# Kernel tuning notes

Measured on AMD Instinct MI355X. Metric: run time of the kernel, lower is better.

## Reference

```python
import jax, jax.numpy as jnp
import numpy as np

X_GRID, Y_GRID = 192, 132
HW = X_GRID * Y_GRID            # 25344
NUM_PROP = 500
NUM_CLS = 6
RADIUS = 10
L_WIN = (2 * RADIUS + 1) ** 2   # 441
D = 128
N_HEADS = 8
D_HEAD = D // N_HEADS
VX, VY = 0.64, 0.64             # feature_map_stride * voxel_size
PC_X0, PC_Y0 = -61.44, -42.24


def _bev_pos():
    # create_2D_grid: linspace(0, size-1, size) + 0.5, meshgrid 'ij', flatten row-major
    bx, by = jnp.meshgrid(jnp.arange(X_GRID, dtype=jnp.float32) + 0.5,
                          jnp.arange(Y_GRID, dtype=jnp.float32) + 0.5, indexing='ij')
    return jnp.stack([bx.reshape(-1), by.reshape(-1)], axis=-1)[None]  # [1, HW, 2]


def conv2d(x, w, b):
    y = jax.lax.conv_general_dilated(x, w, (1, 1), 'SAME',
                                     dimension_numbers=('NCHW', 'OIHW', 'NCHW'))
    return y + b[None, :, None, None]


def maxpool3_valid(x):
    return jax.lax.reduce_window(x, -jnp.inf, jax.lax.max,
                                 (1, 1, 3, 3), (1, 1, 1, 1), 'VALID')


def layer_norm(x, g, b, eps=1e-5):
    m = jnp.mean(x, axis=-1, keepdims=True)
    v = jnp.var(x, axis=-1, keepdims=True)
    return (x - m) * jax.lax.rsqrt(v + eps) * g + b


def pos_emb(p, W1, b1, W2, b2):
    return jax.nn.relu(p @ W1 + b1) @ W2 + b2


def _forward(inputs, W_shared, b_shared, W_hm, b_hm, W_cls, b_cls,
             W_pos1, b_pos1, W_pos2, b_pos2, Wq, bq, Wk, bk, Wv, bv, Wo, bo,
             ln1_g, ln1_b, ln2_g, ln2_b, W_ff1, b_ff1, W_ff2, b_ff2,
             W_center, b_center, W_height, b_height, W_dim, b_dim,
             W_rot, b_rot, W_iou, b_iou, W_hm2, b_hm2):
    x = jnp.transpose(inputs, (0, 1, 3, 2))          # [B,C,192,132]
    B = x.shape[0]
    lidar_feat = jax.nn.relu(conv2d(x, W_shared, b_shared))   # [B,128,192,132]
    lff = lidar_feat.reshape(B, D, HW)

    dense_heatmap = conv2d(lidar_feat, W_hm, b_hm)            # [B,6,192,132]
    heatmap = jax.nn.sigmoid(jax.lax.stop_gradient(dense_heatmap))  # detached in original

    # local-max NMS: 3x3 maxpool on inner region, zeros at border; classes 3..5 bypass NMS
    inner = maxpool3_valid(heatmap)
    local_max = jnp.pad(inner, ((0, 0), (0, 0), (1, 1), (1, 1)))
    local_max = local_max.at[:, 3:6].set(heatmap[:, 3:6])
    hm = heatmap * (heatmap == local_max)

    # threshold + top-k proposals (replaces nonzero+pad+MySortImpe plugin)
    hm_flat = hm.reshape(B, NUM_CLS * HW)
    vals = jnp.where(hm_flat > 0.01, hm_flat, 0.0)
    _, top = jax.lax.top_k(vals, NUM_PROP)            # [B,500]
    cls = top // HW
    sp = top % HW

    query_feat = jnp.take_along_axis(lff, sp[:, None, :], axis=2)  # [B,128,500]
    oh = jax.nn.one_hot(cls, NUM_CLS, dtype=lff.dtype)             # [B,500,6]
    query_feat = query_feat + jnp.einsum('bpc,oc->bop', oh, W_cls) + b_cls[None, :, None]

    bev_pos = jnp.broadcast_to(_bev_pos(), (B, HW, 2))
    query_pos = jnp.take_along_axis(bev_pos, sp[:, :, None], axis=1)  # [B,500,2]

    # windowed key indices (faithful to original //x_grid, %y_grid arithmetic)
    rng = jnp.arange(-RADIUS, RADIUS + 1)
    rx, ry = jnp.meshgrid(rng, rng, indexing='ij')
    kx = (sp // X_GRID)[:, :, None, None] + rx[None, None]
    ky = (sp % Y_GRID)[:, :, None, None] + ry[None, None]
    key_idx = kx.reshape(B, NUM_PROP, L_WIN) * X_GRID + ky.reshape(B, NUM_PROP, L_WIN)
    key_mask = (key_idx < 0) | (key_idx >= HW)
    key_idx = jnp.clip(key_idx, 0, HW - 1)

    key_feat = jnp.take_along_axis(lff, key_idx.reshape(B, 1, -1), axis=2)
    key_feat = key_feat.reshape(B, D, NUM_PROP, L_WIN)
    key_pos = jnp.take_along_axis(bev_pos, key_idx.reshape(B, -1, 1), axis=1)
    key_pos = key_pos.reshape(B, NUM_PROP, L_WIN, 2)

    # decoder: cross-attention of each proposal over its 441-key window
    N = B * NUM_PROP
    q = query_feat.transpose(0, 2, 1).reshape(N, D)
    k = key_feat.transpose(0, 2, 3, 1).reshape(N, L_WIN, D)
    mask = key_mask.reshape(N, L_WIN)
    qpe = pos_emb(query_pos.reshape(N, 2), W_pos1, b_pos1, W_pos2, b_pos2)
    kpe = pos_emb(key_pos.reshape(N, L_WIN, 2), W_pos1, b_pos1, W_pos2, b_pos2)

    qh = ((q + qpe) @ Wq + bq).reshape(N, N_HEADS, D_HEAD)
    kh = ((k + kpe) @ Wk + bk).reshape(N, L_WIN, N_HEADS, D_HEAD)
    vh = (k @ Wv + bv).reshape(N, L_WIN, N_HEADS, D_HEAD)
    scores = jnp.einsum('nhd,nlhd->nhl', qh, kh) / np.float32(np.sqrt(D_HEAD))
    scores = jnp.where(mask[:, None, :], jnp.float32(-1e9), scores)
    attn = jax.nn.softmax(scores, axis=-1)
    ctx = jnp.einsum('nhl,nlhd->nhd', attn, vh).reshape(N, D)
    x1 = layer_norm(q + ctx @ Wo + bo, ln1_g, ln1_b)
    ff = jax.nn.relu(x1 @ W_ff1 + b_ff1) @ W_ff2 + b_ff2
    x2 = layer_norm(x1 + ff, ln2_g, ln2_b)

    qf = x2.reshape(B, NUM_PROP, D).transpose(0, 2, 1)   # [B,128,500]
    head = lambda W, b: jnp.einsum('bcp,oc->bop', qf, W) + b[None, :, None]
    center = head(W_center, b_center) + query_pos.transpose(0, 2, 1)
    height = head(W_height, b_height)
    dim = head(W_dim, b_dim)
    rot = head(W_rot, b_rot)
    iou = head(W_iou, b_iou)
    hm2 = head(W_hm2, b_hm2)

    # get_bboxes / decode_bbox
    score = jax.nn.sigmoid(hm2)                          # [B,6,500]
    _ = (iou + 1.0) * 0.5                                # computed, unused (as in original)
    final_preds = jnp.argmax(score, axis=1).astype(score.dtype)
    final_scores = jnp.max(score, axis=1)
    cx = center[:, 0:1] * VX + PC_X0
    cy = center[:, 1:2] * VY + PC_Y0
    dim = jnp.exp(dim)
    height = height - dim[:, 2:3] * 0.5
    rot = jnp.arctan(rot[:, 0:1] / (rot[:, 1:2] + 1e-6))
    box = jnp.concatenate([cx, cy, height, dim, rot,
                           final_preds[:, None, :], final_scores[:, None, :]], axis=1)
    return box.transpose(0, 2, 1)                        # [B,500,9]


def setup_inputs() -> dict:
    key = jax.random.key(0)
    ks = jax.random.split(key, 20)
    r = lambda k, shape, s=0.02: jax.random.normal(k, shape, dtype=jnp.float32) * s
    z = lambda n: jnp.zeros((n,), dtype=jnp.float32)
    o = lambda n: jnp.ones((n,), dtype=jnp.float32)
    return {
        'inputs': jax.random.normal(ks[0], (1, 256, 132, 192), dtype=jnp.float32),
        'W_shared': r(ks[1], (128, 256, 3, 3)), 'b_shared': z(128),
        'W_hm': r(ks[2], (6, 128, 3, 3)), 'b_hm': z(6),
        'W_cls': r(ks[3], (128, 6)), 'b_cls': z(128),
        'W_pos1': r(ks[4], (2, 128)), 'b_pos1': z(128),
        'W_pos2': r(ks[5], (128, 128)), 'b_pos2': z(128),
        'Wq': r(ks[6], (128, 128)), 'bq': z(128),
        'Wk': r(ks[7], (128, 128)), 'bk': z(128),
        'Wv': r(ks[8], (128, 128)), 'bv': z(128),
        'Wo': r(ks[9], (128, 128)), 'bo': z(128),
        'ln1_g': o(128), 'ln1_b': z(128),
        'ln2_g': o(128), 'ln2_b': z(128),
        'W_ff1': r(ks[10], (128, 256)), 'b_ff1': z(256),
        'W_ff2': r(ks[11], (256, 128)), 'b_ff2': z(128),
        'W_center': r(ks[12], (2, 128)), 'b_center': z(2),
        'W_height': r(ks[13], (1, 128)), 'b_height': z(1),
        'W_dim': r(ks[14], (3, 128)), 'b_dim': z(3),
        'W_rot': r(ks[15], (2, 128)), 'b_rot': z(2),
        'W_iou': r(ks[16], (1, 128)), 'b_iou': z(1),
        'W_hm2': r(ks[17], (6, 128)), 'b_hm2': z(6),
    }


def reference(inputs, W_shared, b_shared, W_hm, b_hm, W_cls, b_cls,
              W_pos1, b_pos1, W_pos2, b_pos2, Wq, bq, Wk, bk, Wv, bv, Wo, bo,
              ln1_g, ln1_b, ln2_g, ln2_b, W_ff1, b_ff1, W_ff2, b_ff2,
              W_center, b_center, W_height, b_height, W_dim, b_dim,
              W_rot, b_rot, W_iou, b_iou, W_hm2, b_hm2):
    return _forward(inputs, W_shared, b_shared, W_hm, b_hm, W_cls, b_cls,
                    W_pos1, b_pos1, W_pos2, b_pos2, Wq, bq, Wk, bk, Wv, bv, Wo, bo,
                    ln1_g, ln1_b, ln2_g, ln2_b, W_ff1, b_ff1, W_ff2, b_ff2,
                    W_center, b_center, W_height, b_height, W_dim, b_dim,
                    W_rot, b_rot, W_iou, b_iou, W_hm2, b_hm2)
```

## Files before the change

kernel.cpp:

```cpp
#include <hip/hip_runtime.h>
#include <math.h>
#include <float.h>

#define XG 192
#define YG 132
#define HW 25344
#define NCLS 6
#define NPROP 500
#define LWIN 441
#define CAP 2048

static __device__ __forceinline__ int imin(int a,int b){return a<b?a:b;}
static __device__ __forceinline__ int imax(int a,int b){return a>b?a:b;}

__device__ __forceinline__ void gl_lds16(const float* gp, float* lp){
  __builtin_amdgcn_global_load_lds(
      (const __attribute__((address_space(1))) unsigned int*)gp,
      (__attribute__((address_space(3))) unsigned int*)lp,
      16, 0, 0);
}

__global__ __launch_bounds__(256) void k_wt(const float* __restrict__ Ws,
                                            const float* __restrict__ Whm,
                                            const float* __restrict__ Wq,
                                            const float* __restrict__ Wp2,
                                            const float* __restrict__ Wo,
                                            const float* __restrict__ Wf1,
                                            const float* __restrict__ Wf2,
                                            float* __restrict__ WT,
                                            float* __restrict__ W6,
                                            float* __restrict__ WQT,
                                            float* __restrict__ WP2T,
                                            float* __restrict__ WOT,
                                            float* __restrict__ WF1T,
                                            float* __restrict__ WF2T,
                                            int* __restrict__ Z){
  int t = blockIdx.x*256 + threadIdx.x;
  if (t < 294912){
    int oc = t & 127, m = t >> 7;
    WT[t] = Ws[(size_t)oc*2304 + m];
  }
  if (t < 6912){
    int c = t & 127, row = t >> 7;
    int cls = row / 9, tap = row % 9;
    W6[t] = Whm[(size_t)cls*1152 + c*9 + tap];
  }
  if (t < 16384){
    int k = t & 127, c = t >> 7;
    WQT[t]  = Wq [(size_t)k*128 + c];
    WP2T[t] = Wp2[(size_t)k*128 + c];
    WOT[t]  = Wo [(size_t)k*128 + c];
  }
  if (t < 32768){
    { int k = t & 127, o = t >> 7;  WF1T[t] = Wf1[(size_t)k*256 + o]; }
    { int k = t & 255, c = t >> 8;  WF2T[t] = Wf2[(size_t)k*128 + c]; }
  }
  if (t < 65568) Z[t] = 0;
}

__global__ __launch_bounds__(256, 4) void k_conv1(const float* __restrict__ IN,
                                                  const float* __restrict__ WT,
                                                  float* __restrict__ O0, float* __restrict__ O1,
                                                  float* __restrict__ O2, float* __restrict__ O3){
  const int b  = blockIdx.x;
  const int g  = blockIdx.y;
  const int i0 = (b % 3) * 64;
  const int j  = b / 3;
  const int tid = threadIdx.x;
  const int wv  = tid >> 6;
  const int oc0 = (tid & 31) * 4;
  const int pxs = tid >> 5;
  __shared__ float wlds[4608];
  __shared__ float hlds[816];
  float4 acc[8];
  #pragma unroll
  for (int px=0;px<8;++px) acc[px] = make_float4(0.f,0.f,0.f,0.f);
  const int C0g = g*64;
  for (int q=0; q<16; ++q){
    __syncthreads();
    const float* wchunk = WT + (size_t)(C0g + q*4)*1152;
    #pragma unroll
    for (int r=0; r<4; ++r)
      gl_lds16(wchunk + (size_t)(r*256 + tid)*4, wlds + (size_t)(r*256 + wv*64)*4);
    if (wv < 2)
      gl_lds16(wchunk + (size_t)(1024 + tid)*4, wlds + (size_t)(1024 + wv*64)*4);
    for (int e=tid; e<792; e+=256){
      int cc = e/198, rem = e%198, r = rem/66, ii = rem%66;
      int gj = j-1+r, gi = i0-1+ii;
      float v = 0.f;
      if ((unsigned)gj < 132u && (unsigned)gi < 192u)
        v = IN[(size_t)(C0g+q*4+cc)*25344 + gj*192 + gi];
      hlds[cc*204 + r*68 + ii] = v;
    }
    __syncthreads();
    for (int cc=0; cc<4; ++cc){
      const float* hb = hlds + cc*204 + pxs*8;
      const float* wb = wlds + cc*1152 + oc0;
      float a[3][10];
      #pragma unroll
      for (int r=0;r<3;++r)
        #pragma unroll
        for (int v=0; v<10; ++v) a[r][v] = hb[r*68 + v];
      #pragma unroll
      for (int kh=0;kh<3;++kh){
        #pragma unroll
        for (int kw=0;kw<3;++kw){
          float4 w = *(const float4*)(wb + (kh*3+kw)*128);
          #pragma unroll
          for (int px=0;px<8;++px){
            float act = a[kw][px+kh];
            acc[px].x += act*w.x;
            acc[px].y += act*w.y;
            acc[px].z += act*w.z;
            acc[px].w += act*w.w;
          }
        }
      }
    }
  }
  float* dst = (g==0)?O0:((g==1)?O1:((g==2)?O2:O3));
  #pragma unroll
  for (int px=0;px<8;++px){
    int p = (i0 + pxs*8 + px)*132 + j;
    *(float4*)(dst + (size_t)p*128 + oc0) = acc[px];
  }
}

__global__ __launch_bounds__(256) void k_cadd(float* __restrict__ LFF,
                                              const float* __restrict__ P1,
                                              const float* __restrict__ P2,
                                              const float* __restrict__ P3,
                                              const float* __restrict__ bias){
  int t = blockIdx.x*256 + threadIdx.x;
  float4 a = ((const float4*)LFF)[t];
  float4 b = ((const float4*)P1)[t];
  float4 c = ((const float4*)P2)[t];
  float4 d = ((const float4*)P3)[t];
  float4 bs = ((const float4*)bias)[t & 31];
  float4 r;
  r.x = fmaxf(a.x+b.x+c.x+d.x+bs.x, 0.f);
  r.y = fmaxf(a.y+b.y+c.y+d.y+bs.y, 0.f);
  r.z = fmaxf(a.z+b.z+c.z+d.z+bs.z, 0.f);
  r.w = fmaxf(a.w+b.w+c.w+d.w+bs.w, 0.f);
  ((float4*)LFF)[t] = r;
}

__global__ __launch_bounds__(256) void k_mid(const float* __restrict__ LFF,
                                             const float* __restrict__ W1, const float* __restrict__ b1,
                                             const float* __restrict__ W2, const float* __restrict__ b2,
                                             const float* __restrict__ Wk, const float* __restrict__ bk,
                                             const float* __restrict__ Wv, const float* __restrict__ bv,
                                             float* __restrict__ KK, float* __restrict__ VV,
                                             const float* __restrict__ W6, const float* __restrict__ bhm,
                                             float* __restrict__ HMS){
  __shared__ float smem[12288];
  const int tid = threadIdx.x;
  const int wv4 = tid >> 6;
  if (blockIdx.x < 792){
    float* hs   = smem;
    float* sf   = smem + 4096;
    float* wbuf = smem + 8192;
    const int p0 = blockIdx.x*32;
    for (int e=tid; e<4096; e+=256){
      int k = e>>5, px = e&31;
      int p = p0+px;
      float bx = (float)(p/132)+0.5f, by = (float)(p%132)+0.5f;
      hs[k*32+px] = fmaxf(bx*W1[k] + by*W1[128+k] + b1[k], 0.f);
    }
    for (int e=tid; e<4096; e+=256){
      int px = e>>7, k = e&127;
      sf[k*32+px] = LFF[(size_t)(p0+px)*128 + k];
    }
    const int pxg = tid & 15, ocg = tid >> 4;
    const int px0 = pxg*2, oc0 = ocg*8;
    float accA[2][8];
    #pragma unroll
    for (int r=0;r<2;++r)
      #pragma unroll
      for (int u=0;u<8;++u) accA[r][u]=0.f;
    for (int c0=0; c0<128; c0+=32){
      __syncthreads();
      const float* wsrc = W2 + (size_t)c0*128;
      #pragma unroll
      for (int r=0;r<4;++r)
        gl_lds16(wsrc + (size_t)(r*256+tid)*4, wbuf + (size_t)(r*256+wv4*64)*4);
      __syncthreads();
      #pragma unroll 2
      for (int k=0;k<32;++k){
        float a0 = hs[(c0+k)*32+px0], a1 = hs[(c0+k)*32+px0+1];
        const float4* w = (const float4*)(wbuf + (size_t)k*128 + oc0);
        float4 w0 = w[0], w1 = w[1];
        accA[0][0]+=a0*w0.x; accA[0][1]+=a0*w0.y; accA[0][2]+=a0*w0.z; accA[0][3]+=a0*w0.w;
        accA[0][4]+=a0*w1.x; accA[0][5]+=a0*w1.y; accA[0][6]+=a0*w1.z; accA[0][7]+=a0*w1.w;
        accA[1][0]+=a1*w0.x; accA[1][1]+=a1*w0.y; accA[1][2]+=a1*w0.z; accA[1][3]+=a1*w0.w;
        accA[1][4]+=a1*w1.x; accA[1][5]+=a1*w1.y; accA[1][6]+=a1*w1.z; accA[1][7]+=a1*w1.w;
      }
    }
    __syncthreads();
    #pragma unroll
    for (int u=0;u<8;++u){
      float bb = b2[oc0+u];
      hs[(oc0+u)*32+px0]   = sf[(oc0+u)*32+px0]   + accA[0][u] + bb;
      hs[(oc0+u)*32+px0+1] = sf[(oc0+u)*32+px0+1] + accA[1][u] + bb;
    }
    float accK[2][8], accV[2][8];
    #pragma unroll
    for (int u=0;u<8;++u){
      float k0 = bk[oc0+u], v0 = bv[oc0+u];
      accK[0][u]=k0; accK[1][u]=k0; accV[0][u]=v0; accV[1][u]=v0;
    }
    for (int c0=0; c0<128; c0+=16){
      __syncthreads();
      #pragma unroll
      for (int r=0;r<2;++r){
        gl_lds16(Wk + (size_t)c0*128 + (size_t)(r*256+tid)*4, wbuf + (size_t)(r*256+wv4*64)*4);
        gl_lds16(Wv + (size_t)c0*128 + (size_t)(r*256+tid)*4, wbuf + 2048 + (size_t)(r*256+wv4*64)*4);
      }
      __syncthreads();
      #pragma unroll 2
      for (int k=0;k<16;++k){
        int kk = c0+k;
        float s0 = hs[kk*32+px0], s1 = hs[kk*32+px0+1];
        float f0 = sf[kk*32+px0], f1 = sf[kk*32+px0+1];
        const float4* wkp = (const float4*)(wbuf + (size_t)k*128 + oc0);
        const float4* wvp = (const float4*)(wbuf + 2048 + (size_t)k*128 + oc0);
        float4 k0v = wkp[0], k1v = wkp[1], v0v = wvp[0], v1v = wvp[1];
        accK[0][0]+=s0*k0v.x; accK[0][1]+=s0*k0v.y; accK[0][2]+=s0*k0v.z; accK[0][3]+=s0*k0v.w;
        accK[0][4]+=s0*k1v.x; accK[0][5]+=s0*k1v.y; accK[0][6]+=s0*k1v.z; accK[0][7]+=s0*k1v.w;
        accK[1][0]+=s1*k0v.x; accK[1][1]+=s1*k0v.y; accK[1][2]+=s1*k0v.z; accK[1][3]+=s1*k0v.w;
        accK[1][4]+=s1*k1v.x; accK[1][5]+=s1*k1v.y; accK[1][6]+=s1*k1v.z; accK[1][7]+=s1*k1v.w;
        accV[0][0]+=f0*v0v.x; accV[0][1]+=f0*v0v.y; accV[0][2]+=f0*v0v.z; accV[0][3]+=f0*v0v.w;
        accV[0][4]+=f0*v1v.x; accV[0][5]+=f0*v1v.y; accV[0][6]+=f0*v1v.z; accV[0][7]+=f0*v1v.w;
        accV[1][0]+=f1*v0v.x; accV[1][1]+=f1*v0v.y; accV[1][2]+=f1*v0v.z; accV[1][3]+=f1*v0v.w;
        accV[1][4]+=f1*v1v.x; accV[1][5]+=f1*v1v.y; accV[1][6]+=f1*v1v.z; accV[1][7]+=f1*v1v.w;
      }
    }
    #pragma unroll
    for (int r=0;r<2;++r){
      int p = p0+px0+r;
      float4* oK = (float4*)(KK + (size_t)p*128 + oc0);
      float4* oV = (float4*)(VV + (size_t)p*128 + oc0);
      float4 t0, t1;
      t0.x=accK[r][0]; t0.y=accK[r][1]; t0.z=accK[r][2]; t0.w=accK[r][3];
      t1.x=accK[r][4]; t1.y=accK[r][5]; t1.z=accK[r][6]; t1.w=accK[r][7];
      oK[0]=t0; oK[1]=t1;
      t0.x=accV[r][0]; t0.y=accV[r][1]; t0.z=accV[r][2]; t0.w=accV[r][3];
      t1.x=accV[r][4]; t1.y=accV[r][5]; t1.z=accV[r][6]; t1.w=accV[r][7];
      oV[0]=t0; oV[1]=t1;
    }
  } else {
    float* w6s = smem;
    float* red = smem + 8192;
    for (int e=tid; e<6912; e+=256) w6s[e] = W6[e];
    __syncthreads();
    int lane = tid & 63, wave = tid >> 6;
    int p = (blockIdx.x - 792)*64 + lane;
    int i = p/132, j = p%132;
    float acc[6] = {0.f,0.f,0.f,0.f,0.f,0.f};
    int cbase = wave*32;
    #pragma unroll
    for (int kh=0; kh<3; ++kh){
      int gi = i+kh-1;
      if ((unsigned)gi >= 192u) continue;
      #pragma unroll
      for (int kw=0; kw<3; ++kw){
        int gj = j+kw-1;
        if ((unsigned)gj >= 132u) continue;
        const float* row = LFF + (size_t)(gi*132+gj)*128 + cbase;
        int tap = kh*3+kw;
        #pragma unroll
        for (int cq=0; cq<8; ++cq){
          float4 v = *(const float4*)(row + cq*4);
          #pragma unroll
          for (int cls=0; cls<6; ++cls){
            float4 wv = *(const float4*)(w6s + (size_t)(cls*9+tap)*128 + cbase + cq*4);
            acc[cls] += v.x*wv.x + v.y*wv.y + v.z*wv.z + v.w*wv.w;
          }
        }
      }
    }
    __syncthreads();
    #pragma unroll
    for (int c=0;c<6;++c) red[(wave*6+c)*64 + lane] = acc[c];
    __syncthreads();
    if (wave==0){
      #pragma unroll
      for (int c=0;c<6;++c){
        float s = red[c*64+lane] + red[(6+c)*64+lane] + red[(12+c)*64+lane] + red[(18+c)*64+lane] + bhm[c];
        HMS[(size_t)c*HW + p] = 1.f/(1.f+expf(-s));
      }
    }
  }
}

__global__ __launch_bounds__(256) void k_nms(const float* __restrict__ HMS,
                                             float* __restrict__ VALS,
                                             int* __restrict__ HIST){
  int t = blockIdx.x*256 + threadIdx.x;
  int c = t / HW, p = t % HW;
  int i = p/132, j = p%132;
  float h = HMS[t];
  float v;
  if (c < 3){
    v = 0.f;
    if (i>=1 && i<=190 && j>=1 && j<=130){
      float m = -1e30f;
      #pragma unroll
      for (int di=-1;di<=1;++di)
        #pragma unroll
        for (int dj=-1;dj<=1;++dj)
          m = fmaxf(m, HMS[(size_t)c*HW + (i+di)*132 + (j+dj)]);
      if (h == m) v = h;
    }
  } else v = h;
  if (!(v > 0.01f)) v = 0.f;
  VALS[t] = v;
  if (v > 0.f) atomicAdd(HIST + (__float_as_uint(v)>>16), 1);
}

__global__ __launch_bounds__(1024) void k_scan(const int* __restrict__ HIST, int* __restrict__ SCAN){
  __shared__ int part[1024];
  __shared__ int gsel;
  int t = threadIdx.x;
  int s = 0, base = t*64;
  for (int u=0;u<64;++u) s += HIST[base+u];
  part[t] = s;
  __syncthreads();
  for (int off=1; off<1024; off<<=1){
    int add = (t+off < 1024) ? part[t+off] : 0;
    __syncthreads();
    part[t] += add;
    __syncthreads();
  }
  int total = part[0];
  int mineI = part[t];
  int nextI = (t < 1023) ? part[t+1] : 0;
  if (mineI >= NPROP && nextI < NPROP) gsel = t;
  if (t == 0 && total < NPROP) gsel = -1;
  __syncthreads();
  int g = gsel;
  if (g < 0){
    if (t==0){ SCAN[0] = 0; SCAN[1] = total; }
    return;
  }
  int cumG = (g < 1023) ? part[g+1] : 0;
  if (t < 64){
    int x = HIST[g*64 + t];
    #pragma unroll
    for (int off=1; off<64; off<<=1){
      int y = __shfl_down(x, off);
      x += (t + off < 64) ? y : 0;
    }
    int Snext = __shfl_down(x, 1);
    int incl  = cumG + x;
    int nextc = (t==63) ? cumG : cumG + Snext;
    if (incl >= NPROP && nextc < NPROP){
      SCAN[0] = g*64 + t;
      SCAN[1] = nextc;
    }
  }
}

__global__ __launch_bounds__(256) void k_collect(const float* __restrict__ VALS,
                                                 const int* __restrict__ SCAN,
                                                 int* __restrict__ CNT,
                                                 float* __restrict__ CV, int* __restrict__ CI){
  int t = blockIdx.x*256 + threadIdx.x;
  float v = VALS[t];
  int bstar = SCAN[0];
  if (v > 0.f && (int)(__float_as_uint(v)>>16) >= bstar){
    int pos = atomicAdd(CNT, 1);
    if (pos < CAP){ CV[pos] = v; CI[pos] = t; }
  }
}

__global__ __launch_bounds__(1024) void k_sort(const float* __restrict__ CV, const int* __restrict__ CI,
                                               const int* __restrict__ CNT,
                                               int* __restrict__ TOPS, int* __restrict__ TOPC){
  __shared__ float sv[CAP];
  __shared__ int   si[CAP];
  int tid = threadIdx.x;
  int M = imin(CNT[0], CAP);
  for (int i=tid; i<CAP; i+=1024){
    if (i < M){ sv[i] = CV[i]; si[i] = CI[i]; }
    else      { sv[i] = -1.f;  si[i] = 0x7fffffff; }
  }
  __syncthreads();
  for (int k=2; k<=CAP; k<<=1){
    for (int j=k>>1; j>0; j>>=1){
      for (int i=tid; i<CAP; i+=1024){
        int p = i ^ j;
        if (p > i){
          bool up = ((i & k) == 0);
          float va = sv[i], vb = sv[p];
          int ia = si[i], ib = si[p];
          bool aFirst = (va > vb) || (va == vb && ia < ib);
          bool bFirst = (vb > va) || (vb == va && ib < ia);
          bool doswap = up ? bFirst : aFirst;
          if (doswap){ sv[i]=vb; sv[p]=va; si[i]=ib; si[p]=ia; }
        }
      }
      __syncthreads();
    }
  }
  for (int t=tid; t<NPROP; t+=1024){
    int idx = imin(si[t], NCLS*HW - 1);
    TOPC[t] = idx / HW;
    TOPS[t] = idx % HW;
  }
}

__global__ __launch_bounds__(256) void k_attn(const float* __restrict__ KK, const float* __restrict__ VV,
                                              const float* __restrict__ LFF,
                                              const int* __restrict__ TOPS, const int* __restrict__ TOPC,
                                              const float* __restrict__ Wcls, const float* __restrict__ bcls,
                                              const float* __restrict__ pW1, const float* __restrict__ pb1,
                                              const float* __restrict__ WP2T, const float* __restrict__ pb2,
                                              const float* __restrict__ WQT, const float* __restrict__ bq,
                                              const float* __restrict__ WOT, const float* __restrict__ bo,
                                              const float* __restrict__ g1, const float* __restrict__ b1,
                                              const float* __restrict__ WF1T, const float* __restrict__ bf1,
                                              const float* __restrict__ WF2T, const float* __restrict__ bf2,
                                              const float* __restrict__ g2, const float* __restrict__ b2,
                                              const float* __restrict__ Wc, const float* __restrict__ bc,
                                              const float* __restrict__ Wh, const float* __restrict__ bh,
                                              const float* __restrict__ Wd, const float* __restrict__ bd,
                                              const float* __restrict__ Wr, const float* __restrict__ br,
                                              const float* __restrict__ Whm2, const float* __restrict__ bhm2,
                                              float* __restrict__ out){
  int n = blockIdx.x, tid = threadIdx.x;
  __shared__ __align__(16) float qhL[128];
  __shared__ float sc[8*441];
  __shared__ int   kiL[441];
  __shared__ __align__(16) float ctxL[128];
  __shared__ float xL[128];
  __shared__ float hidL[256];
  __shared__ float sumsL[8];
  __shared__ float stat[2];
  __shared__ float dots[16];
  int sp = TOPS[n];
  int cls = TOPC[n];
  const int kb64 = (tid>>7)*64, c128 = tid&127;
  float qreg = 0.f;
  if (tid < 128){
    float qx = (float)(sp/132)+0.5f, qy = (float)(sp%132)+0.5f;
    ctxL[tid] = fmaxf(qx*pW1[tid] + qy*pW1[128+tid] + pb1[tid], 0.f);
    qreg = LFF[(size_t)sp*128+tid] + Wcls[tid*6+cls] + bcls[tid];
  }
  __syncthreads();
  {
    const float4* wp = (const float4*)(WP2T + (size_t)c128*128 + kb64);
    float pe = 0.f;
    #pragma unroll
    for (int k4=0;k4<16;++k4){
      float4 w = wp[k4]; int kb = kb64 + k4*4;
      pe += ctxL[kb]*w.x + ctxL[kb+1]*w.y + ctxL[kb+2]*w.z + ctxL[kb+3]*w.w;
    }
    sc[tid] = pe;
  }
  __syncthreads();
  if (tid < 128) xL[tid] = qreg + pb2[tid] + sc[tid] + sc[tid+128];
  __syncthreads();
  {
    const float4* wp = (const float4*)(WQT + (size_t)c128*128 + kb64);
    float qh = 0.f;
    #pragma unroll
    for (int k4=0;k4<16;++k4){
      float4 w = wp[k4]; int kb = kb64 + k4*4;
      qh += xL[kb]*w.x + xL[kb+1]*w.y + xL[kb+2]*w.z + xL[kb+3]*w.w;
    }
    sc[tid] = qh;
  }
  __syncthreads();
  if (tid < 128) qhL[tid] = bq[tid] + sc[tid] + sc[tid+128];
  __syncthreads();
  int spx = sp/192, spy = sp%132;
  for (int l = tid; l < 441; l += 256){
    int a = l/21, bb = l%21;
    int kidx = (spx + a - 10)*192 + (spy + bb - 10);
    bool msk = (kidx < 0) || (kidx >= HW);
    int kc = imin(imax(kidx,0), HW-1);
    kiL[l] = kc;
    const float4* kk4 = (const float4*)(KK + (size_t)kc*128);
    const float4* qh4 = (const float4*)qhL;
    #pragma unroll
    for (int hh=0; hh<8; ++hh){
      float acc = 0.f;
      #pragma unroll
      for (int d4=0; d4<4; ++d4){
        float4 kv = kk4[hh*4+d4]; float4 qv = qh4[hh*4+d4];
        acc += kv.x*qv.x + kv.y*qv.y + kv.z*qv.z + kv.w*qv.w;
      }
      sc[hh*441+l] = msk ? -1e9f : acc*0.25f;
    }
  }
  __syncthreads();
  int wave = tid>>6, lane = tid&63;
  for (int hh = wave; hh < 8; hh += 4){
    float mx = -3.0e38f;
    for (int l = lane; l < 441; l += 64) mx = fmaxf(mx, sc[hh*441+l]);
    #pragma unroll
    for (int off=32; off; off>>=1) mx = fmaxf(mx, __shfl_xor(mx, off));
    float sum = 0.f;
    for (int l = lane; l < 441; l += 64){
      float e = __expf(sc[hh*441+l] - mx);
      sc[hh*441+l] = e; sum += e;
    }
    #pragma unroll
    for (int off=32; off; off>>=1) sum += __shfl_xor(sum, off);
    if (lane==0) sumsL[hh] = sum;
  }
  __syncthreads();
  for (int hh = wave; hh < 8; hh += 4){
    float a[16];
    #pragma unroll
    for (int d=0; d<16; ++d) a[d]=0.f;
    for (int l = lane; l < 441; l += 64){
      float w = sc[hh*441+l];
      const float4* vv4 = (const float4*)(VV + (size_t)kiL[l]*128 + hh*16);
      #pragma unroll
      for (int d4=0; d4<4; ++d4){
        float4 v = vv4[d4];
        a[d4*4+0]+=w*v.x; a[d4*4+1]+=w*v.y; a[d4*4+2]+=w*v.z; a[d4*4+3]+=w*v.w;
      }
    }
    #pragma unroll
    for (int d=0; d<16; ++d){
      #pragma unroll
      for (int off=32; off; off>>=1) a[d] += __shfl_xor(a[d], off);
    }
    if (lane==0){
      float inv = 1.f/sumsL[hh];
      #pragma unroll
      for (int d=0; d<16; ++d) ctxL[hh*16+d] = a[d]*inv;
    }
  }
  __syncthreads();
  {
    const float4* wp = (const float4*)(WOT + (size_t)c128*128 + kb64);
    float acc = 0.f;
    #pragma unroll
    for (int k4=0;k4<16;++k4){
      float4 w = wp[k4]; int kb = kb64 + k4*4;
      acc += ctxL[kb]*w.x + ctxL[kb+1]*w.y + ctxL[kb+2]*w.z + ctxL[kb+3]*w.w;
    }
    sc[tid] = acc;
  }
  __syncthreads();
  float x1v = 0.f;
  if (tid < 128){
    x1v = qreg + bo[tid] + sc[tid] + sc[tid+128];
    xL[tid] = x1v;
  }
  __syncthreads();
  if (tid < 64){
    float u0 = xL[tid], u1 = xL[tid+64];
    float s = u0+u1, s2 = u0*u0+u1*u1;
    #pragma unroll
    for (int off=32; off; off>>=1){ s += __shfl_xor(s, off); s2 += __shfl_xor(s2, off); }
    if (tid==0){ float mean = s*(1.f/128.f); float var = s2*(1.f/128.f) - mean*mean;
      stat[0]=mean; stat[1]=rsqrtf(var + 1e-5f); }
  }
  __syncthreads();
  if (tid < 128) xL[tid] = (x1v - stat[0])*stat[1]*g1[tid] + b1[tid];
  __syncthreads();
  {
    const float4* wp = (const float4*)(WF1T + (size_t)tid*128);
    float hv = bf1[tid];
    #pragma unroll 8
    for (int k4=0;k4<32;++k4){
      float4 w = wp[k4]; int kb = k4*4;
      hv += xL[kb]*w.x + xL[kb+1]*w.y + xL[kb+2]*w.z + xL[kb+3]*w.w;
    }
    hidL[tid] = fmaxf(hv, 0.f);
  }
  __syncthreads();
  {
    int kb0 = (tid>>7)*128;
    const float4* wp = (const float4*)(WF2T + (size_t)c128*256 + kb0);
    float acc = 0.f;
    #pragma unroll 8
    for (int k4=0;k4<32;++k4){
      float4 w = wp[k4]; int kb = kb0 + k4*4;
      acc += hidL[kb]*w.x + hidL[kb+1]*w.y + hidL[kb+2]*w.z + hidL[kb+3]*w.w;
    }
    sc[tid] = acc;
  }
  __syncthreads();
  float x2v = 0.f;
  if (tid < 128) x2v = xL[tid] + bf2[tid] + sc[tid] + sc[tid+128];
  __syncthreads();
  if (tid < 128) hidL[tid] = x2v;
  __syncthreads();
  if (tid < 64){
    float u0 = hidL[tid], u1 = hidL[tid+64];
    float s = u0+u1, s2 = u0*u0+u1*u1;
    #pragma unroll
    for (int off=32; off; off>>=1){ s += __shfl_xor(s, off); s2 += __shfl_xor(s2, off); }
    if (tid==0){ float mean = s*(1.f/128.f); float var = s2*(1.f/128.f) - mean*mean;
      stat[0]=mean; stat[1]=rsqrtf(var + 1e-5f); }
  }
  __syncthreads();
  if (tid < 128) xL[tid] = (x2v - stat[0])*stat[1]*g2[tid] + b2[tid];
  __syncthreads();
  if (tid < 14){
    const float* Wp; float bb;
    if (tid < 2)      { Wp = Wc + tid*128;        bb = bc[tid];      }
    else if (tid < 3) { Wp = Wh;                  bb = bh[0];        }
    else if (tid < 6) { Wp = Wd + (tid-3)*128;    bb = bd[tid-3];    }
    else if (tid < 8) { Wp = Wr + (tid-6)*128;    bb = br[tid-6];    }
    else              { Wp = Whm2 + (tid-8)*128;  bb = bhm2[tid-8];  }
    float acc = bb;
    for (int k=0;k<128;++k) acc += xL[k]*Wp[k];
    dots[tid] = acc;
  }
  __syncthreads();
  if (tid == 0){
    float qpx = (float)(sp/132)+0.5f, qpy = (float)(sp%132)+0.5f;
    float cx = (dots[0]+qpx)*0.64f - 61.44f;
    float cy = (dots[1]+qpy)*0.64f - 42.24f;
    float e0 = expf(dots[3]), e1 = expf(dots[4]), e2 = expf(dots[5]);
    float hgt = dots[2] - e2*0.5f;
    float rot = atanf(dots[6]/(dots[7] + 1e-6f));
    float bestv = -1.f; int bestc = 0;
    #pragma unroll
    for (int m=0;m<6;++m){
      float s = 1.f/(1.f + expf(-dots[8+m]));
      if (s > bestv){ bestv = s; bestc = m; }
    }
    float* o = out + (size_t)n*9;
    o[0]=cx; o[1]=cy; o[2]=hgt; o[3]=e0; o[4]=e1; o[5]=e2; o[6]=rot;
    o[7]=(float)bestc; o[8]=bestv;
  }
}

extern "C" void kernel_launch(void* const* d_in, const int* in_sizes, int n_in,
                              void* d_out, int out_size, void* d_ws, size_t ws_size,
                              hipStream_t stream){
  (void)in_sizes; (void)n_in; (void)out_size;
  const float* IN   = (const float*)d_in[0];
  const float* Wsh  = (const float*)d_in[1];
  const float* bsh  = (const float*)d_in[2];
  const float* Whm  = (const float*)d_in[3];
  const float* bhm  = (const float*)d_in[4];
  const float* Wcls = (const float*)d_in[5];
  const float* bcls = (const float*)d_in[6];
  const float* Wp1  = (const float*)d_in[7];
  const float* bp1  = (const float*)d_in[8];
  const float* Wp2  = (const float*)d_in[9];
  const float* bp2  = (const float*)d_in[10];
  const float* Wq   = (const float*)d_in[11];
  const float* bq   = (const float*)d_in[12];
  const float* Wk   = (const float*)d_in[13];
  const float* bk   = (const float*)d_in[14];
  const float* Wv   = (const float*)d_in[15];
  const float* bv   = (const float*)d_in[16];
  const float* Wo   = (const float*)d_in[17];
  const float* bo   = (const float*)d_in[18];
  const float* g1   = (const float*)d_in[19];
  const float* b1   = (const float*)d_in[20];
  const float* g2   = (const float*)d_in[21];
  const float* b2   = (const float*)d_in[22];
  const float* Wf1  = (const float*)d_in[23];
  const float* bf1  = (const float*)d_in[24];
  const float* Wf2  = (const float*)d_in[25];
  const float* bf2  = (const float*)d_in[26];
  const float* Wc   = (const float*)d_in[27];
  const float* bc   = (const float*)d_in[28];
  const float* Wh   = (const float*)d_in[29];
  const float* bh   = (const float*)d_in[30];
  const float* Wd   = (const float*)d_in[31];
  const float* bd   = (const float*)d_in[32];
  const float* Wr   = (const float*)d_in[33];
  const float* br   = (const float*)d_in[34];
  const float* Whm2 = (const float*)d_in[37];
  const float* bhm2 = (const float*)d_in[38];
  float* out = (float*)d_out;
  float* W = (float*)d_ws;

  const size_t N_LFF  = (size_t)HW*128;
  const size_t OFF_LFF  = 0;
  const size_t OFF_PE   = OFF_LFF + N_LFF;
  const size_t OFF_KK   = OFF_PE + N_LFF;
  const size_t OFF_VV   = OFF_KK + N_LFF;
  const size_t OFF_WT   = OFF_VV + N_LFF;
  const size_t OFF_WHMT = OFF_WT + 294912;
  const size_t OFF_HMS  = OFF_WHMT + 6912;
  const size_t OFF_VALS = OFF_HMS + 152064;
  const size_t OFF_HIST = OFF_VALS + 152064;
  const size_t OFF_SCAN = OFF_HIST + 65536;
  const size_t OFF_CNT  = OFF_SCAN + 16;
  const size_t OFF_CV   = OFF_CNT + 16;
  const size_t OFF_CI   = OFF_CV + CAP;
  const size_t OFF_TOPS = OFF_CI + CAP;
  const size_t OFF_TOPC = OFF_TOPS + 512;
  const size_t OFF_WQT  = OFF_TOPC + 512;
  const size_t OFF_WP2T = OFF_WQT + 16384;
  const size_t OFF_WOT  = OFF_WP2T + 16384;
  const size_t OFF_WF1T = OFF_WOT + 16384;
  const size_t OFF_WF2T = OFF_WF1T + 32768;
  const size_t TOTAL    = OFF_WF2T + 32768;
  if (ws_size < TOTAL*sizeof(float)) return;

  k_wt    <<<1152, 256, 0, stream>>>(Wsh, Whm, Wq, Wp2, Wo, Wf1, Wf2,
                                     W+OFF_WT, W+OFF_WHMT,
                                     W+OFF_WQT, W+OFF_WP2T, W+OFF_WOT, W+OFF_WF1T, W+OFF_WF2T,
                                     (int*)(W+OFF_HIST));
  k_conv1 <<<dim3(396,4), 256, 0, stream>>>(IN, W+OFF_WT, W+OFF_LFF, W+OFF_PE, W+OFF_KK, W+OFF_VV);
  k_cadd  <<<3168, 256, 0, stream>>>(W+OFF_LFF, W+OFF_PE, W+OFF_KK, W+OFF_VV, bsh);
  k_mid   <<<1188, 256, 0, stream>>>(W+OFF_LFF, Wp1, bp1, Wp2, bp2, Wk, bk, Wv, bv,
                                     W+OFF_KK, W+OFF_VV, W+OFF_WHMT, bhm, W+OFF_HMS);
  k_nms   <<<594,  256, 0, stream>>>(W+OFF_HMS, W+OFF_VALS, (int*)(W+OFF_HIST));
  k_scan  <<<1,   1024, 0, stream>>>((const int*)(W+OFF_HIST), (int*)(W+OFF_SCAN));
  k_collect<<<594, 256, 0, stream>>>(W+OFF_VALS, (const int*)(W+OFF_SCAN),
                                     (int*)(W+OFF_CNT), W+OFF_CV, (int*)(W+OFF_CI));
  k_sort  <<<1,   1024, 0, stream>>>(W+OFF_CV, (const int*)(W+OFF_CI), (const int*)(W+OFF_CNT),
                                     (int*)(W+OFF_TOPS), (int*)(W+OFF_TOPC));
  k_attn  <<<500,  256, 0, stream>>>(W+OFF_KK, W+OFF_VV, W+OFF_LFF,
                                     (const int*)(W+OFF_TOPS), (const int*)(W+OFF_TOPC),
                                     Wcls, bcls, Wp1, bp1, W+OFF_WP2T, bp2, W+OFF_WQT, bq,
                                     W+OFF_WOT, bo, g1, b1, W+OFF_WF1T, bf1, W+OFF_WF2T, bf2, g2, b2,
                                     Wc, bc, Wh, bh, Wd, bd, Wr, br, Whm2, bhm2, out);
}
```

Baseline: 583.3 us.

## Run shared 3x3 conv on bf16 MFMA with three-way split precision

Replaces the FP32 FMA direct convolution, which was split over four channel groups with partial sums, with one implicit-GEMM kernel on bf16 MFMA 16x16x32 instructions. Inputs and weights are each split into three bf16 parts, and six cross-product MFMAs per tile keep accuracy close to FP32. Bias and ReLU are fused into the epilogue, which removes the separate partial-sum add kernel and the three extra HW×128 buffers. In exchange it adds activation splitting inside the kernel, more block-level syncs per channel chunk and tap, and lower occupancy.

```diff
diff --git a/kernel.cpp b/kernel.cpp
--- a/kernel.cpp
+++ b/kernel.cpp
@@ -10,6 +10,10 @@
 #define LWIN 441
 #define CAP 2048
 
+typedef unsigned short ushort_t;
+typedef __attribute__((ext_vector_type(8))) short bf8v;
+typedef __attribute__((ext_vector_type(4))) float f4v;
+
 static __device__ __forceinline__ int imin(int a,int b){return a<b?a:b;}
 static __device__ __forceinline__ int imax(int a,int b){return a>b?a:b;}
 
@@ -18,6 +22,20 @@
       (const __attribute__((address_space(1))) unsigned int*)gp,
       (__attribute__((address_space(3))) unsigned int*)lp,
       16, 0, 0);
+}
+__device__ __forceinline__ void gl_lds16u(const ushort_t* gp, ushort_t* lp){
+  __builtin_amdgcn_global_load_lds(
+      (const __attribute__((address_space(1))) unsigned int*)gp,
+      (__attribute__((address_space(3))) unsigned int*)lp,
+      16, 0, 0);
+}
+
+__device__ __forceinline__ ushort_t f2bf(float x){
+  unsigned u = __float_as_uint(x);
+  return (ushort_t)((u + 0x7FFFu + ((u>>16)&1u)) >> 16);
+}
+__device__ __forceinline__ float bf2f(ushort_t h){
+  return __uint_as_float(((unsigned)h)<<16);
 }
 
 __global__ __launch_bounds__(256) void k_wt(const float* __restrict__ Ws,
@@ -27,18 +45,32 @@
                                             const float* __restrict__ Wo,
                                             const float* __restrict__ Wf1,
                                             const float* __restrict__ Wf2,
-                                            float* __restrict__ WT,
                                             float* __restrict__ W6,
                                             float* __restrict__ WQT,
                                             float* __restrict__ WP2T,
                                             float* __restrict__ WOT,
                                             float* __restrict__ WF1T,
                                             float* __restrict__ WF2T,
+                                            ushort_t* __restrict__ BQ0,
+                                            ushort_t* __restrict__ BQ1,
+                                            ushort_t* __restrict__ BQ2,
                                             int* __restrict__ Z){
   int t = blockIdx.x*256 + threadIdx.x;
   if (t < 294912){
-    int oc = t & 127, m = t >> 7;
-    WT[t] = Ws[(size_t)oc*2304 + m];
+    int kl = t & 31;
+    int rest = t >> 5;
+    int n = rest & 127;
+    int tc = rest >> 7;
+    int tap = tc >> 3, chunk = tc & 7;
+    int c = chunk*32 + kl;
+    float v = Ws[(size_t)n*2304 + c*9 + tap];
+    ushort_t h0 = f2bf(v);
+    float r1 = v - bf2f(h0);
+    ushort_t h1 = f2bf(r1);
+    float r2 = r1 - bf2f(h1);
+    ushort_t h2 = f2bf(r2);
+    size_t dst = (size_t)tc*5120 + n*40 + kl;
+    BQ0[dst] = h0; BQ1[dst] = h1; BQ2[dst] = h2;
   }
   if (t < 6912){
     int c = t & 127, row = t >> 7;
@@ -58,91 +90,130 @@
   if (t < 65568) Z[t] = 0;
 }
 
-__global__ __launch_bounds__(256, 4) void k_conv1(const float* __restrict__ IN,
-                                                  const float* __restrict__ WT,
-                                                  float* __restrict__ O0, float* __restrict__ O1,
-                                                  float* __restrict__ O2, float* __restrict__ O3){
+__global__ __launch_bounds__(256, 3) void k_conv1(const float* __restrict__ IN,
+                                                  const ushort_t* __restrict__ BQ0,
+                                                  const ushort_t* __restrict__ BQ1,
+                                                  const ushort_t* __restrict__ BQ2,
+                                                  const float* __restrict__ bias,
+                                                  float* __restrict__ LFF){
   const int b  = blockIdx.x;
-  const int g  = blockIdx.y;
   const int i0 = (b % 3) * 64;
   const int j  = b / 3;
   const int tid = threadIdx.x;
-  const int wv  = tid >> 6;
-  const int oc0 = (tid & 31) * 4;
-  const int pxs = tid >> 5;
-  __shared__ float wlds[4608];
-  __shared__ float hlds[816];
-  float4 acc[8];
+  const int w    = tid >> 6;
+  const int lane = tid & 63;
+  const int l15  = lane & 15, quad = lane >> 4;
+  __shared__ __align__(16) ushort_t SM[23280];
+  ushort_t* As0 = SM;
+  ushort_t* As1 = SM + 2640;
+  ushort_t* As2 = SM + 5280;
+  ushort_t* Bs0 = SM + 7920;
+  ushort_t* Bs1 = SM + 13040;
+  ushort_t* Bs2 = SM + 18160;
+  f4v acc[4][2];
   #pragma unroll
-  for (int px=0;px<8;++px) acc[px] = make_float4(0.f,0.f,0.f,0.f);
-  const int C0g = g*64;
-  for (int q=0; q<16; ++q){
-    __syncthreads();
-    const float* wchunk = WT + (size_t)(C0g + q*4)*1152;
-    #pragma unroll
-    for (int r=0; r<4; ++r)
-      gl_lds16(wchunk + (size_t)(r*256 + tid)*4, wlds + (size_t)(r*256 + wv*64)*4);
-    if (wv < 2)
-      gl_lds16(wchunk + (size_t)(1024 + tid)*4, wlds + (size_t)(1024 + wv*64)*4);
-    for (int e=tid; e<792; e+=256){
-      int cc = e/198, rem = e%198, r = rem/66, ii = rem%66;
-      int gj = j-1+r, gi = i0-1+ii;
-      float v = 0.f;
-      if ((unsigned)gj < 132u && (unsigned)gi < 192u)
-        v = IN[(size_t)(C0g+q*4+cc)*25344 + gj*192 + gi];
-      hlds[cc*204 + r*68 + ii] = v;
-    }
-    __syncthreads();
-    for (int cc=0; cc<4; ++cc){
-      const float* hb = hlds + cc*204 + pxs*8;
-      const float* wb = wlds + cc*1152 + oc0;
-      float a[3][10];
-      #pragma unroll
-      for (int r=0;r<3;++r)
-        #pragma unroll
-        for (int v=0; v<10; ++v) a[r][v] = hb[r*68 + v];
-      #pragma unroll
-      for (int kh=0;kh<3;++kh){
-        #pragma unroll
-        for (int kw=0;kw<3;++kw){
-          float4 w = *(const float4*)(wb + (kh*3+kw)*128);
-          #pragma unroll
-          for (int px=0;px<8;++px){
-            float act = a[kw][px+kh];
-            acc[px].x += act*w.x;
-            acc[px].y += act*w.y;
-            acc[px].z += act*w.z;
-            acc[px].w += act*w.w;
+  for (int mq=0;mq<4;++mq)
+    #pragma unroll
+    for (int nt=0;nt<2;++nt) acc[mq][nt] = (f4v){0.f,0.f,0.f,0.f};
+
+  for (int chunk=0; chunk<8; ++chunk){
+    for (int kw=0; kw<3; ++kw){
+      __syncthreads();
+      {
+        int gj = j - 1 + kw;
+        bool jok = (unsigned)gj < 132u;
+        for (int e = tid; e < 2112; e += 256){
+          int c = e / 66, ii = e - c*66;
+          int gi = i0 - 1 + ii;
+          float v = 0.f;
+          if (jok && (unsigned)gi < 192u)
+            v = IN[(size_t)(chunk*32 + c)*25344 + gj*192 + gi];
+          ushort_t h0 = f2bf(v);
+          float r1 = v - bf2f(h0);
+          ushort_t h1 = f2bf(r1);
+          float r2 = r1 - bf2f(h1);
+          ushort_t h2 = f2bf(r2);
+          int a = ii*40 + c;
+          As0[a] = h0; As1[a] = h1; As2[a] = h2;
+        }
+      }
+      for (int kh=0; kh<3; ++kh){
+        if (kh > 0) __syncthreads();
+        {
+          int tc = (kh*3 + kw)*8 + chunk;
+          const ushort_t* s0 = BQ0 + (size_t)tc*5120;
+          const ushort_t* s1 = BQ1 + (size_t)tc*5120;
+          const ushort_t* s2 = BQ2 + (size_t)tc*5120;
+          gl_lds16u(s0 + (size_t)tid*8,       Bs0 + (size_t)(w*64)*8);
+          gl_lds16u(s0 + (size_t)(256+tid)*8, Bs0 + (size_t)(256 + w*64)*8);
+          gl_lds16u(s1 + (size_t)tid*8,       Bs1 + (size_t)(w*64)*8);
+          gl_lds16u(s1 + (size_t)(256+tid)*8, Bs1 + (size_t)(256 + w*64)*8);
+          gl_lds16u(s2 + (size_t)tid*8,       Bs2 + (size_t)(w*64)*8);
+          gl_lds16u(s2 + (size_t)(256+tid)*8, Bs2 + (size_t)(256 + w*64)*8);
+          if (tid < 128){
+            gl_lds16u(s0 + (size_t)(512+tid)*8, Bs0 + (size_t)(512 + w*64)*8);
+            gl_lds16u(s1 + (size_t)(512+tid)*8, Bs1 + (size_t)(512 + w*64)*8);
+            gl_lds16u(s2 + (size_t)(512+tid)*8, Bs2 + (size_t)(512 + w*64)*8);
           }
         }
-      }
-    }
-  }
-  float* dst = (g==0)?O0:((g==1)?O1:((g==2)?O2:O3));
+        __syncthreads();
+        bf8v A0[4], A1[4], A2[4];
+        #pragma unroll
+        for (int mq=0; mq<4; ++mq){
+          int off = (mq*16 + l15 + kh)*40 + quad*8;
+          A0[mq] = *(const bf8v*)&As0[off];
+          A1[mq] = *(const bf8v*)&As1[off];
+          A2[mq] = *(const bf8v*)&As2[off];
+        }
+        bf8v B0[2], B1[2], B2[2];
+        #pragma unroll
+        for (int ntl=0; ntl<2; ++ntl){
+          int off = ((w*2+ntl)*16 + l15)*40 + quad*8;
+          B0[ntl] = *(const bf8v*)&Bs0[off];
+          B1[ntl] = *(const bf8v*)&Bs1[off];
+          B2[ntl] = *(const bf8v*)&Bs2[off];
+        }
+        #pragma unroll
+        for (int mq=0;mq<4;++mq){
+          #pragma unroll
+          for (int ntl=0;ntl<2;++ntl){
+            f4v c = acc[mq][ntl];
+            c = __builtin_amdgcn_mfma_f32_16x16x32_bf16(A0[mq], B0[ntl], c, 0,0,0);
+            c = __builtin_amdgcn_mfma_f32_16x16x32_bf16(A0[mq], B1[ntl], c, 0,0,0);
+            c = __builtin_amdgcn_mfma_f32_16x16x32_bf16(A1[mq], B0[ntl], c, 0,0,0);
+            c = __builtin_amdgcn_mfma_f32_16x16x32_bf16(A0[mq], B2[ntl], c, 0,0,0);
+            c = __builtin_amdgcn_mfma_f32_16x16x32_bf16(A1[mq], B1[ntl], c, 0,0,0);
+            c = __builtin_amdgcn_mfma_f32_16x16x32_bf16(A2[mq], B0[ntl], c, 0,0,0);
+            acc[mq][ntl] = c;
+          }
+        }
+      }
+    }
+  }
+  __syncthreads();
+  float* Cs = (float*)SM;
   #pragma unroll
-  for (int px=0;px<8;++px){
-    int p = (i0 + pxs*8 + px)*132 + j;
-    *(float4*)(dst + (size_t)p*128 + oc0) = acc[px];
-  }
-}
-
-__global__ __launch_bounds__(256) void k_cadd(float* __restrict__ LFF,
-                                              const float* __restrict__ P1,
-                                              const float* __restrict__ P2,
-                                              const float* __restrict__ P3,
-                                              const float* __restrict__ bias){
-  int t = blockIdx.x*256 + threadIdx.x;
-  float4 a = ((const float4*)LFF)[t];
-  float4 b = ((const float4*)P1)[t];
-  float4 c = ((const float4*)P2)[t];
-  float4 d = ((const float4*)P3)[t];
-  float4 bs = ((const float4*)bias)[t & 31];
-  float4 r;
-  r.x = fmaxf(a.x+b.x+c.x+d.x+bs.x, 0.f);
-  r.y = fmaxf(a.y+b.y+c.y+d.y+bs.y, 0.f);
-  r.z = fmaxf(a.z+b.z+c.z+d.z+bs.z, 0.f);
-  r.w = fmaxf(a.w+b.w+c.w+d.w+bs.w, 0.f);
-  ((float4*)LFF)[t] = r;
+  for (int mq=0;mq<4;++mq)
+    #pragma unroll
+    for (int ntl=0;ntl<2;++ntl)
+      #pragma unroll
+      for (int r=0;r<4;++r){
+        int m = mq*16 + quad*4 + r;
+        int oc = (w*2+ntl)*16 + l15;
+        Cs[m*128 + oc] = acc[mq][ntl][r];
+      }
+  __syncthreads();
+  for (int e = tid; e < 2048; e += 256){
+    int m = e >> 5, ocq = e & 31;
+    float4 v = *(float4*)&Cs[m*128 + ocq*4];
+    float4 bs = *(const float4*)&bias[ocq*4];
+    v.x = fmaxf(v.x + bs.x, 0.f);
+    v.y = fmaxf(v.y + bs.y, 0.f);
+    v.z = fmaxf(v.z + bs.z, 0.f);
+    v.w = fmaxf(v.w + bs.w, 0.f);
+    int p = (i0 + m)*132 + j;
+    *(float4*)&LFF[(size_t)p*128 + ocq*4] = v;
+  }
 }
 
 __global__ __launch_bounds__(256) void k_mid(const float* __restrict__ LFF,
@@ -680,12 +751,10 @@
 
   const size_t N_LFF  = (size_t)HW*128;
   const size_t OFF_LFF  = 0;
-  const size_t OFF_PE   = OFF_LFF + N_LFF;
-  const size_t OFF_KK   = OFF_PE + N_LFF;
+  const size_t OFF_KK   = OFF_LFF + N_LFF;
   const size_t OFF_VV   = OFF_KK + N_LFF;
-  const size_t OFF_WT   = OFF_VV + N_LFF;
-  const size_t OFF_WHMT = OFF_WT + 294912;
-  const size_t OFF_HMS  = OFF_WHMT + 6912;
+  const size_t OFF_W6   = OFF_VV + N_LFF;
+  const size_t OFF_HMS  = OFF_W6 + 6912;
   const size_t OFF_VALS = OFF_HMS + 152064;
   const size_t OFF_HIST = OFF_VALS + 152064;
   const size_t OFF_SCAN = OFF_HIST + 65536;
@@ -699,17 +768,24 @@
   const size_t OFF_WOT  = OFF_WP2T + 16384;
   const size_t OFF_WF1T = OFF_WOT + 16384;
   const size_t OFF_WF2T = OFF_WF1T + 32768;
-  const size_t TOTAL    = OFF_WF2T + 32768;
+  const size_t OFF_BQ0  = OFF_WF2T + 32768;
+  const size_t OFF_BQ1  = OFF_BQ0 + 184320;
+  const size_t OFF_BQ2  = OFF_BQ1 + 184320;
+  const size_t TOTAL    = OFF_BQ2 + 184320;
   if (ws_size < TOTAL*sizeof(float)) return;
 
+  ushort_t* BQ0 = (ushort_t*)(W + OFF_BQ0);
+  ushort_t* BQ1 = (ushort_t*)(W + OFF_BQ1);
+  ushort_t* BQ2 = (ushort_t*)(W + OFF_BQ2);
+
   k_wt    <<<1152, 256, 0, stream>>>(Wsh, Whm, Wq, Wp2, Wo, Wf1, Wf2,
-                                     W+OFF_WT, W+OFF_WHMT,
+                                     W+OFF_W6,
                                      W+OFF_WQT, W+OFF_WP2T, W+OFF_WOT, W+OFF_WF1T, W+OFF_WF2T,
+                                     BQ0, BQ1, BQ2,
                                      (int*)(W+OFF_HIST));
-  k_conv1 <<<dim3(396,4), 256, 0, stream>>>(IN, W+OFF_WT, W+OFF_LFF, W+OFF_PE, W+OFF_KK, W+OFF_VV);
-  k_cadd  <<<3168, 256, 0, stream>>>(W+OFF_LFF, W+OFF_PE, W+OFF_KK, W+OFF_VV, bsh);
+  k_conv1 <<<396, 256, 0, stream>>>(IN, BQ0, BQ1, BQ2, bsh, W+OFF_LFF);
   k_mid   <<<1188, 256, 0, stream>>>(W+OFF_LFF, Wp1, bp1, Wp2, bp2, Wk, bk, Wv, bv,
-                                     W+OFF_KK, W+OFF_VV, W+OFF_WHMT, bhm, W+OFF_HMS);
+                                     W+OFF_KK, W+OFF_VV, W+OFF_W6, bhm, W+OFF_HMS);
   k_nms   <<<594,  256, 0, stream>>>(W+OFF_HMS, W+OFF_VALS, (int*)(W+OFF_HIST));
   k_scan  <<<1,   1024, 0, stream>>>((const int*)(W+OFF_HIST), (int*)(W+OFF_SCAN));
   k_collect<<<594, 256, 0, stream>>>(W+OFF_VALS, (const int*)(W+OFF_SCAN),
```

New measurement: 543.1 us. 1.07x faster.
